# Kernel tuning notes

Hardware: AMD Instinct MI355X
Metric: run time of the kernel (lower is better)

## Reference

```python
import jax, jax.numpy as jnp
import numpy as np

N = 50000          # nodes
E = 800000         # edges (before self-loops)
F_IN = 256         # feature_dim
HEADS = 3
OUT = 128          # per-head channels
HO = HEADS * OUT   # 384
NUM_GRAPHS = 64
NUM_CLASSES = 2
SLOPE = 0.2        # PyG GATConv default negative_slope


def setup_inputs() -> dict:
    key = jax.random.key(0)
    ks = jax.random.split(key, 8)
    x = jax.random.normal(ks[0], (N, F_IN), dtype=jnp.float32)
    edge_index = jax.random.randint(ks[1], (2, E), 0, N)
    batch = jnp.sort(jax.random.randint(ks[2], (N,), 0, NUM_GRAPHS))
    # GATConv params (glorot-ish scales)
    W = jax.random.normal(ks[3], (F_IN, HO), dtype=jnp.float32) * (1.0 / np.sqrt(F_IN))
    att_src = jax.random.normal(ks[4], (HEADS, OUT), dtype=jnp.float32) * 0.1
    att_dst = jax.random.normal(ks[5], (HEADS, OUT), dtype=jnp.float32) * 0.1
    bias = jnp.zeros((HO,), dtype=jnp.float32)
    fc_w = jax.random.normal(ks[6], (HO, NUM_CLASSES), dtype=jnp.float32) * 0.05
    fc_b = jnp.zeros((NUM_CLASSES,), dtype=jnp.float32)
    return {"x": x, "edge_index": edge_index, "batch": batch, "W": W,
            "att_src": att_src, "att_dst": att_dst, "bias": bias,
            "fc_w": fc_w, "fc_b": fc_b}


def reference(x, edge_index, batch, W, att_src, att_dst, bias, fc_w, fc_b):
    n = x.shape[0]
    h = (x @ W).reshape(n, HEADS, OUT)                      # [N, H, C]
    # add self-loops (PyG default add_self_loops=True)
    loops = jnp.arange(n)
    src = jnp.concatenate([edge_index[0], loops])           # [E+N]
    dst = jnp.concatenate([edge_index[1], loops])
    # per-node attention logits
    a_src = jnp.einsum('nhc,hc->nh', h, att_src)            # [N, H]
    a_dst = jnp.einsum('nhc,hc->nh', h, att_dst)
    e = jax.nn.leaky_relu(a_src[src] + a_dst[dst], SLOPE)   # [E+N, H]
    # segment softmax over incoming edges of each dst node
    emax = jax.ops.segment_max(e, dst, num_segments=n)
    ex = jnp.exp(e - emax[dst])
    denom = jax.ops.segment_sum(ex, dst, num_segments=n)
    alpha = ex / (denom[dst] + 1e-16)                       # [E+N, H]
    # weighted scatter-add aggregation
    msg = h[src] * alpha[:, :, None]                        # [E+N, H, C]
    out = jax.ops.segment_sum(msg, dst, num_segments=n)     # [N, H, C]
    out = jax.nn.relu(out.reshape(n, HO) + bias)            # [N, 384]
    # global mean pool per graph
    counts = jax.ops.segment_sum(jnp.ones((n,), out.dtype), batch,
                                 num_segments=NUM_GRAPHS)
    pooled = jax.ops.segment_sum(out, batch, num_segments=NUM_GRAPHS)
    pooled = pooled / jnp.maximum(counts, 1.0)[:, None]     # [G, 384]
    return pooled @ fc_w + fc_b                             # [G, num_classes]
```

## Files before the change

kernel.cpp:

```cpp
#include <hip/hip_runtime.h>
#include <hip/hip_bf16.h>
#include <math.h>

#define HEADS 3
#define HO 384
#define NGRAPH 64
#define F_IN 256
#define SLOPE 0.2f

typedef __attribute__((ext_vector_type(8))) short bf8;
typedef __attribute__((ext_vector_type(4))) float f4;

__device__ __forceinline__ unsigned short bfr(float f) {
    unsigned u = __float_as_uint(f);
    u += 0x7fffu + ((u >> 16) & 1u);
    return (unsigned short)(u >> 16);
}
__device__ __forceinline__ float bflo(unsigned u) { return __uint_as_float(u << 16); }
__device__ __forceinline__ float bfhi(unsigned u) { return __uint_as_float(u & 0xffff0000u); }
__device__ __forceinline__ float lrelu(float v) { return (v > 0.f) ? v : SLOPE * v; }

__global__ __launch_bounds__(256) void misc_k(const int* __restrict__ ei,
                                              const float* __restrict__ W,
                                              const int* __restrict__ batch,
                                              int* __restrict__ count,
                                              int* __restrict__ rank,
                                              short* __restrict__ WbT,
                                              int* __restrict__ gstart,
                                              int NBc, int E, int N) {
    int b = blockIdx.x;
    if (b < NBc) {
        int e = b * 256 + threadIdx.x;
        int ET = E + N;
        if (e >= ET) return;
        int d = (e < E) ? ei[E + e] : (e - E);
        rank[e] = atomicAdd(&count[d], 1);
    } else if (b < NBc + 384) {
        int n = b - NBc;
        int k = threadIdx.x;
        WbT[n * 256 + k] = (short)bfr(W[(size_t)k * HO + n]);
    } else {
        int g = threadIdx.x;
        if (g > NGRAPH) return;
        int lo = 0, hi = N;
        while (lo < hi) { int mid = (lo + hi) >> 1; if (batch[mid] < g) lo = mid + 1; else hi = mid; }
        gstart[g] = lo;
    }
}

#define XS_STRIDE 40
__global__ __launch_bounds__(256, 3) void gemm_att(const float* __restrict__ X,
                                                   const short* __restrict__ WbT,
                                                   const float* __restrict__ att_src,
                                                   const float* __restrict__ att_dst,
                                                   unsigned* __restrict__ Hb,
                                                   float* __restrict__ aSrcO,
                                                   float* __restrict__ aDstO, int N) {
    __shared__ short Xs[64 * XS_STRIDE];
    __shared__ short Bs[384 * XS_STRIDE];
    __shared__ float lsS[64][8];
    __shared__ float lsD[64][8];
    int t = threadIdx.x;
    int w = t >> 6, lane = t & 63;
    int quad = lane >> 4, l15 = lane & 15;
    int rbase = blockIdx.x * 64;

    int sr = t >> 2;
    int sko = (t & 3) * 8;
    int xrow = rbase + sr;
    xrow = (xrow < N) ? xrow : (N - 1);
    const float* xrp = X + (size_t)xrow * F_IN;

    f4 acc[4][6] = {};

    float4 p0 = *(const float4*)(xrp + sko);
    float4 p1 = *(const float4*)(xrp + sko + 4);

    for (int k0 = 0; k0 < F_IN; k0 += 32) {
        __syncthreads();
        {
            bf8 pk;
            pk[0] = (short)bfr(p0.x); pk[1] = (short)bfr(p0.y);
            pk[2] = (short)bfr(p0.z); pk[3] = (short)bfr(p0.w);
            pk[4] = (short)bfr(p1.x); pk[5] = (short)bfr(p1.y);
            pk[6] = (short)bfr(p1.z); pk[7] = (short)bfr(p1.w);
            *(bf8*)(&Xs[sr * XS_STRIDE + sko]) = pk;
        }
#pragma unroll
        for (int i = 0; i < 6; i++) {
            int n = i * 64 + sr;
            bf8 b = *(const bf8*)(WbT + (size_t)n * F_IN + k0 + sko);
            *(bf8*)(&Bs[n * XS_STRIDE + sko]) = b;
        }
        __syncthreads();
        if (k0 + 32 < F_IN) {
            p0 = *(const float4*)(xrp + k0 + 32 + sko);
            p1 = *(const float4*)(xrp + k0 + 32 + sko + 4);
        }
        bf8 ar[4], br[6];
#pragma unroll
        for (int at = 0; at < 4; at++)
            ar[at] = *(const bf8*)(&Xs[(at * 16 + l15) * XS_STRIDE + quad * 8]);
#pragma unroll
        for (int nt = 0; nt < 6; nt++)
            br[nt] = *(const bf8*)(&Bs[(w * 96 + nt * 16 + l15) * XS_STRIDE + quad * 8]);
#pragma unroll
        for (int at = 0; at < 4; at++)
#pragma unroll
            for (int nt = 0; nt < 6; nt++)
                acc[at][nt] = __builtin_amdgcn_mfma_f32_16x16x32_bf16(ar[at], br[nt], acc[at][nt], 0, 0, 0);
    }

    const int splits[4] = {6, 2, 4, 0};
    int split = splits[w];
    float asv[6], adv[6];
#pragma unroll
    for (int nt = 0; nt < 6; nt++) {
        int c = w * 96 + nt * 16 + l15;
        asv[nt] = att_src[c];
        adv[nt] = att_dst[c];
    }
#pragma unroll
    for (int at = 0; at < 4; at++) {
#pragma unroll
        for (int r = 0; r < 4; r++) {
            float paS = 0.f, pbS = 0.f, paD = 0.f, pbD = 0.f;
#pragma unroll
            for (int nt = 0; nt < 6; nt++) {
                float v = acc[at][nt][r];
                if (nt < split) { paS += v * asv[nt]; paD += v * adv[nt]; }
                else            { pbS += v * asv[nt]; pbD += v * adv[nt]; }
            }
#pragma unroll
            for (int off = 1; off < 16; off <<= 1) {
                paS += __shfl_xor(paS, off); pbS += __shfl_xor(pbS, off);
                paD += __shfl_xor(paD, off); pbD += __shfl_xor(pbD, off);
            }
            if (l15 == 0) {
                int row = at * 16 + quad * 4 + r;
                lsS[row][w * 2 + 0] = paS; lsS[row][w * 2 + 1] = pbS;
                lsD[row][w * 2 + 0] = paD; lsD[row][w * 2 + 1] = pbD;
            }
        }
    }
#pragma unroll
    for (int at = 0; at < 4; at++) {
#pragma unroll
        for (int nt = 0; nt < 6; nt++) {
#pragma unroll
            for (int r = 0; r < 4; r++) {
                float v = acc[at][nt][r];
                float vp = __shfl_xor(v, 1);
                int node = rbase + at * 16 + quad * 4 + r;
                if (!(lane & 1) && node < N) {
                    unsigned pk = (unsigned)bfr(v) | ((unsigned)bfr(vp) << 16);
                    Hb[(size_t)node * 192 + w * 48 + nt * 8 + (l15 >> 1)] = pk;
                }
            }
        }
    }
    __syncthreads();
    if (t < 64) {
        int node = rbase + t;
        if (node < N) {
            aSrcO[node * 3 + 0] = lsS[t][0] + lsS[t][2];
            aSrcO[node * 3 + 1] = lsS[t][3] + lsS[t][4];
            aSrcO[node * 3 + 2] = lsS[t][5] + lsS[t][7];
            aDstO[node * 3 + 0] = lsD[t][0] + lsD[t][2];
            aDstO[node * 3 + 1] = lsD[t][3] + lsD[t][4];
            aDstO[node * 3 + 2] = lsD[t][5] + lsD[t][7];
        }
    }
}

__global__ __launch_bounds__(256) void scan_a(const int* __restrict__ count,
                                              int* __restrict__ offsets,
                                              int* __restrict__ bsums, int N) {
    __shared__ int tmp[256];
    int t = threadIdx.x;
    int i = blockIdx.x * 256 + t;
    int v = (i < N) ? count[i] : 0;
    tmp[t] = v;
    __syncthreads();
    for (int off = 1; off < 256; off <<= 1) {
        int x = (t >= off) ? tmp[t - off] : 0;
        __syncthreads();
        tmp[t] += x;
        __syncthreads();
    }
    if (i < N) offsets[i] = tmp[t] - v;
    if (t == 255) bsums[blockIdx.x] = tmp[255];
}

__global__ __launch_bounds__(256) void scan_b(int* __restrict__ bsums, int NB) {
    __shared__ int tmp[256];
    int t = threadIdx.x;
    int v = (t < NB) ? bsums[t] : 0;
    tmp[t] = v;
    __syncthreads();
    for (int off = 1; off < 256; off <<= 1) {
        int x = (t >= off) ? tmp[t - off] : 0;
        __syncthreads();
        tmp[t] += x;
        __syncthreads();
    }
    if (t < NB) bsums[t] = tmp[t] - v;
}

__global__ __launch_bounds__(256) void scan_c(int* __restrict__ offsets,
                                              const int* __restrict__ bsums, int N) {
    int i = blockIdx.x * 256 + threadIdx.x;
    if (i < N) offsets[i] += bsums[blockIdx.x];
}

__global__ __launch_bounds__(256) void scatter_k(const int* __restrict__ ei,
                                                 const int* __restrict__ rank,
                                                 const int* __restrict__ offsets,
                                                 int* __restrict__ csr_src, int E, int N) {
    int e = blockIdx.x * 256 + threadIdx.x;
    int ET = E + N;
    if (e >= ET) return;
    int s, d;
    if (e < E) { s = ei[e]; d = ei[E + e]; } else { s = e - E; d = s; }
    csr_src[offsets[d] + rank[e]] = s;
}

__global__ __launch_bounds__(256) void aggregate_k(const unsigned* __restrict__ Hb,
                                                   const int* __restrict__ csr_src,
                                                   const int* __restrict__ offsets,
                                                   const int* __restrict__ count,
                                                   const float* __restrict__ a_src,
                                                   const float* __restrict__ a_dst,
                                                   const float* __restrict__ bias,
                                                   unsigned* __restrict__ outb, int N) {
    int wid = blockIdx.x * 4 + (threadIdx.x >> 6);
    int lane = threadIdx.x & 63;
    if (wid >= N) return;
    int start = offsets[wid], n = count[wid];
    float ad0 = a_dst[wid * 3 + 0], ad1 = a_dst[wid * 3 + 1], ad2 = a_dst[wid * 3 + 2];
    float a0l = 0.f, a0h = 0.f, a1l = 0.f, a1h = 0.f, a2l = 0.f, a2h = 0.f;

    if (n <= 64) {
        int sreg = 0;
        float l0 = -INFINITY, l1 = -INFINITY, l2 = -INFINITY;
        if (lane < n) {
            sreg = csr_src[start + lane];
            l0 = lrelu(a_src[sreg * 3 + 0] + ad0);
            l1 = lrelu(a_src[sreg * 3 + 1] + ad1);
            l2 = lrelu(a_src[sreg * 3 + 2] + ad2);
        }
        unsigned u0[8], u1[8], u2[8];
#pragma unroll
        for (int q = 0; q < 8; q++) {
            int s = __shfl(sreg, q);
            const unsigned* h = Hb + (size_t)s * 192;
            u0[q] = h[lane]; u1[q] = h[lane + 64]; u2[q] = h[lane + 128];
        }
        float m0 = l0, m1 = l1, m2 = l2;
#pragma unroll
        for (int off = 1; off < 64; off <<= 1) {
            m0 = fmaxf(m0, __shfl_xor(m0, off));
            m1 = fmaxf(m1, __shfl_xor(m1, off));
            m2 = fmaxf(m2, __shfl_xor(m2, off));
        }
        float e0 = (lane < n) ? expf(l0 - m0) : 0.f;
        float e1 = (lane < n) ? expf(l1 - m1) : 0.f;
        float e2 = (lane < n) ? expf(l2 - m2) : 0.f;
        float s0 = e0, s1 = e1, s2 = e2;
#pragma unroll
        for (int off = 1; off < 64; off <<= 1) {
            s0 += __shfl_xor(s0, off);
            s1 += __shfl_xor(s1, off);
            s2 += __shfl_xor(s2, off);
        }
        float i0 = 1.f / (s0 + 1e-16f), i1 = 1.f / (s1 + 1e-16f), i2 = 1.f / (s2 + 1e-16f);
        for (int j = 0; j < n; j += 8) {
            float wq0[8], wq1[8], wq2[8];
#pragma unroll
            for (int q = 0; q < 8; q++) {
                wq0[q] = __shfl(e0, j + q);
                wq1[q] = __shfl(e1, j + q);
                wq2[q] = __shfl(e2, j + q);
            }
#pragma unroll
            for (int q = 0; q < 8; q++) {
                a0l += wq0[q] * bflo(u0[q]); a0h += wq0[q] * bfhi(u0[q]);
                a1l += wq1[q] * bflo(u1[q]); a1h += wq1[q] * bfhi(u1[q]);
                a2l += wq2[q] * bflo(u2[q]); a2h += wq2[q] * bfhi(u2[q]);
            }
            if (j + 8 < n) {
#pragma unroll
                for (int q = 0; q < 8; q++) {
                    int s = __shfl(sreg, j + 8 + q);
                    const unsigned* h = Hb + (size_t)s * 192;
                    u0[q] = h[lane]; u1[q] = h[lane + 64]; u2[q] = h[lane + 128];
                }
            }
        }
        a0l *= i0; a0h *= i0;
        a1l *= i1; a1h *= i1;
        a2l *= i2; a2h *= i2;
    } else {
        float m0 = -INFINITY, m1 = -INFINITY, m2 = -INFINITY;
        for (int j = lane; j < n; j += 64) {
            int s = csr_src[start + j];
            m0 = fmaxf(m0, lrelu(a_src[s * 3 + 0] + ad0));
            m1 = fmaxf(m1, lrelu(a_src[s * 3 + 1] + ad1));
            m2 = fmaxf(m2, lrelu(a_src[s * 3 + 2] + ad2));
        }
#pragma unroll
        for (int off = 1; off < 64; off <<= 1) {
            m0 = fmaxf(m0, __shfl_xor(m0, off));
            m1 = fmaxf(m1, __shfl_xor(m1, off));
            m2 = fmaxf(m2, __shfl_xor(m2, off));
        }
        float s0 = 0.f, s1 = 0.f, s2 = 0.f;
        for (int j = lane; j < n; j += 64) {
            int s = csr_src[start + j];
            s0 += expf(lrelu(a_src[s * 3 + 0] + ad0) - m0);
            s1 += expf(lrelu(a_src[s * 3 + 1] + ad1) - m1);
            s2 += expf(lrelu(a_src[s * 3 + 2] + ad2) - m2);
        }
#pragma unroll
        for (int off = 1; off < 64; off <<= 1) {
            s0 += __shfl_xor(s0, off);
            s1 += __shfl_xor(s1, off);
            s2 += __shfl_xor(s2, off);
        }
        float i0 = 1.f / (s0 + 1e-16f), i1 = 1.f / (s1 + 1e-16f), i2 = 1.f / (s2 + 1e-16f);
        for (int j = 0; j < n; j++) {
            int s = csr_src[start + j];
            float w0 = expf(lrelu(a_src[s * 3 + 0] + ad0) - m0) * i0;
            float w1 = expf(lrelu(a_src[s * 3 + 1] + ad1) - m1) * i1;
            float w2 = expf(lrelu(a_src[s * 3 + 2] + ad2) - m2) * i2;
            const unsigned* h = Hb + (size_t)s * 192;
            unsigned u0 = h[lane], u1 = h[lane + 64], u2 = h[lane + 128];
            a0l += w0 * bflo(u0); a0h += w0 * bfhi(u0);
            a1l += w1 * bflo(u1); a1h += w1 * bfhi(u1);
            a2l += w2 * bflo(u2); a2h += w2 * bfhi(u2);
        }
    }

    unsigned* orow = outb + (size_t)wid * 192;
    int c0 = 2 * lane;
    float b0 = bias[c0], b1 = bias[c0 + 1];
    float b2 = bias[128 + c0], b3 = bias[128 + c0 + 1];
    float b4 = bias[256 + c0], b5 = bias[256 + c0 + 1];
    float v, x0, x1;
    unsigned pk;
    v = a0l + b0; x0 = (v > 0.f) ? v : 0.f;
    v = a0h + b1; x1 = (v > 0.f) ? v : 0.f;
    pk = (unsigned)bfr(x0) | ((unsigned)bfr(x1) << 16);
    orow[lane] = pk;
    v = a1l + b2; x0 = (v > 0.f) ? v : 0.f;
    v = a1h + b3; x1 = (v > 0.f) ? v : 0.f;
    pk = (unsigned)bfr(x0) | ((unsigned)bfr(x1) << 16);
    orow[64 + lane] = pk;
    v = a2l + b4; x0 = (v > 0.f) ? v : 0.f;
    v = a2h + b5; x1 = (v > 0.f) ? v : 0.f;
    pk = (unsigned)bfr(x0) | ((unsigned)bfr(x1) << 16);
    orow[128 + lane] = pk;
}

__global__ __launch_bounds__(192) void pool_k(const unsigned* __restrict__ outb,
                                              const int* __restrict__ gstart,
                                              float* __restrict__ pooled) {
    int g = blockIdx.x;
    int chunk = blockIdx.y;
    int t = threadIdx.x;
    int lo = gstart[g], hi = gstart[g + 1];
    float al = 0.f, ah = 0.f;
    for (int r = lo + chunk; r < hi; r += 8) {
        unsigned u = outb[(size_t)r * 192 + t];
        al += bflo(u);
        ah += bfhi(u);
    }
    atomicAdd(&pooled[g * HO + 2 * t], al);
    atomicAdd(&pooled[g * HO + 2 * t + 1], ah);
}

__global__ __launch_bounds__(64) void fc_k(const float* __restrict__ pooled,
                                           const int* __restrict__ gstart,
                                           const float* __restrict__ fc_w,
                                           const float* __restrict__ fc_b,
                                           float* __restrict__ out) {
    int g = blockIdx.x;
    int lane = threadIdx.x;
    float a0 = 0.f, a1 = 0.f;
#pragma unroll
    for (int k = 0; k < 6; k++) {
        int c = lane + 64 * k;
        float pv = pooled[g * HO + c];
        a0 += pv * fc_w[c * 2 + 0];
        a1 += pv * fc_w[c * 2 + 1];
    }
#pragma unroll
    for (int off = 32; off > 0; off >>= 1) {
        a0 += __shfl_down(a0, off);
        a1 += __shfl_down(a1, off);
    }
    if (lane == 0) {
        float cnt = fmaxf((float)(gstart[g + 1] - gstart[g]), 1.0f);
        out[g * 2 + 0] = a0 / cnt + fc_b[0];
        out[g * 2 + 1] = a1 / cnt + fc_b[1];
    }
}

extern "C" void kernel_launch(void* const* d_in, const int* in_sizes, int n_in,
                              void* d_out, int out_size, void* d_ws, size_t ws_size,
                              hipStream_t stream) {
    const float* x       = (const float*)d_in[0];
    const int*   ei      = (const int*)d_in[1];
    const int*   batch   = (const int*)d_in[2];
    const float* W       = (const float*)d_in[3];
    const float* att_src = (const float*)d_in[4];
    const float* att_dst = (const float*)d_in[5];
    const float* bias    = (const float*)d_in[6];
    const float* fc_w    = (const float*)d_in[7];
    const float* fc_b    = (const float*)d_in[8];
    float* out = (float*)d_out;

    const int N = in_sizes[2];
    const int E = in_sizes[1] / 2;
    const int ET = E + N;

    char* p = (char*)d_ws;
    auto alloc = [&](size_t bytes) -> char* {
        char* r = p;
        p += (bytes + 255) & ~(size_t)255;
        return r;
    };
    short*    wbt    = (short*)alloc((size_t)HO * F_IN * 2);
    unsigned* hb     = (unsigned*)alloc((size_t)N * 192 * 4);
    unsigned* outb   = (unsigned*)alloc((size_t)N * 192 * 4);
    float*    a_src  = (float*)alloc((size_t)N * 3 * 4);
    float*    a_dst  = (float*)alloc((size_t)N * 3 * 4);
    char*     zstart = p;
    int*      count  = (int*)alloc((size_t)N * 4);
    float*    pooled = (float*)alloc((size_t)NGRAPH * HO * 4);
    size_t    zbytes = (size_t)(p - zstart);
    int*      offsets = (int*)alloc((size_t)N * 4);
    int*      rank    = (int*)alloc((size_t)ET * 4);
    int*      bsums   = (int*)alloc(4096);
    int*      gstart  = (int*)alloc(1024);
    int*      csr_src = (int*)alloc((size_t)ET * 4);

    hipMemsetAsync(zstart, 0, zbytes, stream);

    int NBc = (ET + 255) / 256;
    misc_k<<<NBc + 384 + 1, 256, 0, stream>>>(ei, W, batch, count, rank, wbt, gstart,
                                              NBc, E, N);
    gemm_att<<<(N + 63) / 64, 256, 0, stream>>>(x, wbt, att_src, att_dst,
                                                hb, a_src, a_dst, N);
    int NB = (N + 255) / 256;
    scan_a<<<NB, 256, 0, stream>>>(count, offsets, bsums, N);
    scan_b<<<1, 256, 0, stream>>>(bsums, NB);
    scan_c<<<NB, 256, 0, stream>>>(offsets, bsums, N);
    scatter_k<<<(ET + 255) / 256, 256, 0, stream>>>(ei, rank, offsets, csr_src, E, N);
    aggregate_k<<<(N + 3) / 4, 256, 0, stream>>>(hb, csr_src, offsets, count,
                                                 a_src, a_dst, bias, outb, N);
    dim3 pg(NGRAPH, 8);
    pool_k<<<pg, 192, 0, stream>>>(outb, gstart, pooled);
    fc_k<<<NGRAPH, 64, 0, stream>>>(pooled, gstart, fc_w, fc_b, out);

    (void)n_in; (void)out_size; (void)ws_size;
}
```

Measured before the change: 330.0 us.

## Quantize projected node features to int8 with per-node-per-head scales for aggregation

The GEMM epilogue now computes a per-node, per-head absmax and stores the projected features as int8 instead of bf16. The per-head scales are packed alongside the source attention logits in an 8-float record per node. The aggregation kernel gathers half as many bytes per neighbour row, folds the dequant scale into the softmax weight, and writes output with wider vector stores using 48 lanes. This cuts the gather traffic that dominates aggregation, in exchange for int8 quantization error and extra unpack arithmetic per element.

```diff
diff --git a/kernel.cpp b/kernel.cpp
--- a/kernel.cpp
+++ b/kernel.cpp
@@ -10,6 +10,8 @@
 
 typedef __attribute__((ext_vector_type(8))) short bf8;
 typedef __attribute__((ext_vector_type(4))) float f4;
+typedef __attribute__((ext_vector_type(2))) unsigned u2v;
+typedef __attribute__((ext_vector_type(4))) unsigned u4v;
 
 __device__ __forceinline__ unsigned short bfr(float f) {
     unsigned u = __float_as_uint(f);
@@ -19,6 +21,17 @@
 __device__ __forceinline__ float bflo(unsigned u) { return __uint_as_float(u << 16); }
 __device__ __forceinline__ float bfhi(unsigned u) { return __uint_as_float(u & 0xffff0000u); }
 __device__ __forceinline__ float lrelu(float v) { return (v > 0.f) ? v : SLOPE * v; }
+
+__device__ __forceinline__ void dec_fma(float* acc, float wm, unsigned ux, unsigned uy) {
+    acc[0] += wm * (float)((signed char)(ux));
+    acc[1] += wm * (float)((signed char)(ux >> 8));
+    acc[2] += wm * (float)((signed char)(ux >> 16));
+    acc[3] += wm * (float)((signed char)(ux >> 24));
+    acc[4] += wm * (float)((signed char)(uy));
+    acc[5] += wm * (float)((signed char)(uy >> 8));
+    acc[6] += wm * (float)((signed char)(uy >> 16));
+    acc[7] += wm * (float)((signed char)(uy >> 24));
+}
 
 __global__ __launch_bounds__(256) void misc_k(const int* __restrict__ ei,
                                               const float* __restrict__ W,
@@ -53,13 +66,15 @@
                                                    const short* __restrict__ WbT,
                                                    const float* __restrict__ att_src,
                                                    const float* __restrict__ att_dst,
-                                                   unsigned* __restrict__ Hb,
-                                                   float* __restrict__ aSrcO,
+                                                   signed char* __restrict__ hc,
+                                                   float* __restrict__ ni,
                                                    float* __restrict__ aDstO, int N) {
     __shared__ short Xs[64 * XS_STRIDE];
     __shared__ short Bs[384 * XS_STRIDE];
     __shared__ float lsS[64][8];
     __shared__ float lsD[64][8];
+    __shared__ float lsM[64][8];
+    __shared__ float sclS[64][4];
     int t = threadIdx.x;
     int w = t >> 6, lane = t & 63;
     int quad = lane >> 4, l15 = lane & 15;
@@ -146,29 +161,63 @@
 #pragma unroll
     for (int at = 0; at < 4; at++) {
 #pragma unroll
-        for (int nt = 0; nt < 6; nt++) {
-#pragma unroll
-            for (int r = 0; r < 4; r++) {
-                float v = acc[at][nt][r];
-                float vp = __shfl_xor(v, 1);
-                int node = rbase + at * 16 + quad * 4 + r;
-                if (!(lane & 1) && node < N) {
-                    unsigned pk = (unsigned)bfr(v) | ((unsigned)bfr(vp) << 16);
-                    Hb[(size_t)node * 192 + w * 48 + nt * 8 + (l15 >> 1)] = pk;
-                }
+        for (int r = 0; r < 4; r++) {
+            float pa = 0.f, pb = 0.f;
+#pragma unroll
+            for (int nt = 0; nt < 6; nt++) {
+                float v = fabsf(acc[at][nt][r]);
+                if (nt < split) pa = fmaxf(pa, v); else pb = fmaxf(pb, v);
+            }
+#pragma unroll
+            for (int off = 1; off < 16; off <<= 1) {
+                pa = fmaxf(pa, __shfl_xor(pa, off));
+                pb = fmaxf(pb, __shfl_xor(pb, off));
+            }
+            if (l15 == 0) {
+                int row = at * 16 + quad * 4 + r;
+                lsM[row][w * 2 + 0] = pa; lsM[row][w * 2 + 1] = pb;
             }
         }
     }
     __syncthreads();
     if (t < 64) {
+        float s0 = fmaxf(lsM[t][0], lsM[t][2]);
+        float s1 = fmaxf(lsM[t][3], lsM[t][4]);
+        float s2 = fmaxf(lsM[t][5], lsM[t][7]);
+        sclS[t][0] = (s0 > 0.f) ? 127.f / s0 : 0.f;
+        sclS[t][1] = (s1 > 0.f) ? 127.f / s1 : 0.f;
+        sclS[t][2] = (s2 > 0.f) ? 127.f / s2 : 0.f;
         int node = rbase + t;
         if (node < N) {
-            aSrcO[node * 3 + 0] = lsS[t][0] + lsS[t][2];
-            aSrcO[node * 3 + 1] = lsS[t][3] + lsS[t][4];
-            aSrcO[node * 3 + 2] = lsS[t][5] + lsS[t][7];
             aDstO[node * 3 + 0] = lsD[t][0] + lsD[t][2];
             aDstO[node * 3 + 1] = lsD[t][3] + lsD[t][4];
             aDstO[node * 3 + 2] = lsD[t][5] + lsD[t][7];
+            float4 nA, nB;
+            nA.x = lsS[t][0] + lsS[t][2];
+            nA.y = lsS[t][3] + lsS[t][4];
+            nA.z = lsS[t][5] + lsS[t][7];
+            nA.w = s0 / 127.f;
+            nB.x = s1 / 127.f;
+            nB.y = s2 / 127.f;
+            nB.z = 0.f; nB.w = 0.f;
+            *(float4*)(ni + (size_t)node * 8) = nA;
+            *(float4*)(ni + (size_t)node * 8 + 4) = nB;
+        }
+    }
+    __syncthreads();
+#pragma unroll
+    for (int at = 0; at < 4; at++) {
+#pragma unroll
+        for (int nt = 0; nt < 6; nt++) {
+            int hd = (w * 96 + nt * 16) >> 7;
+#pragma unroll
+            for (int r = 0; r < 4; r++) {
+                int row = at * 16 + quad * 4 + r;
+                int node = rbase + row;
+                float rq = sclS[row][hd];
+                int qi = (int)rintf(acc[at][nt][r] * rq);
+                if (node < N) hc[(size_t)node * 384 + w * 96 + nt * 16 + l15] = (signed char)qi;
+            }
         }
     }
 }
@@ -225,11 +274,11 @@
     csr_src[offsets[d] + rank[e]] = s;
 }
 
-__global__ __launch_bounds__(256) void aggregate_k(const unsigned* __restrict__ Hb,
+__global__ __launch_bounds__(256) void aggregate_k(const unsigned* __restrict__ hcw,
                                                    const int* __restrict__ csr_src,
                                                    const int* __restrict__ offsets,
                                                    const int* __restrict__ count,
-                                                   const float* __restrict__ a_src,
+                                                   const float* __restrict__ ni,
                                                    const float* __restrict__ a_dst,
                                                    const float* __restrict__ bias,
                                                    unsigned* __restrict__ outb, int N) {
@@ -238,128 +287,118 @@
     if (wid >= N) return;
     int start = offsets[wid], n = count[wid];
     float ad0 = a_dst[wid * 3 + 0], ad1 = a_dst[wid * 3 + 1], ad2 = a_dst[wid * 3 + 2];
-    float a0l = 0.f, a0h = 0.f, a1l = 0.f, a1h = 0.f, a2l = 0.f, a2h = 0.f;
+    int head_my = lane >> 4;
+    int off = (lane < 48) ? 2 * lane : 0;
+    float acc[8] = {0.f, 0.f, 0.f, 0.f, 0.f, 0.f, 0.f, 0.f};
+    float i0, i1, i2;
 
     if (n <= 64) {
         int sreg = 0;
         float l0 = -INFINITY, l1 = -INFINITY, l2 = -INFINITY;
+        float s0v = 0.f, s1v = 0.f, s2v = 0.f;
         if (lane < n) {
             sreg = csr_src[start + lane];
-            l0 = lrelu(a_src[sreg * 3 + 0] + ad0);
-            l1 = lrelu(a_src[sreg * 3 + 1] + ad1);
-            l2 = lrelu(a_src[sreg * 3 + 2] + ad2);
-        }
-        unsigned u0[8], u1[8], u2[8];
-#pragma unroll
-        for (int q = 0; q < 8; q++) {
-            int s = __shfl(sreg, q);
-            const unsigned* h = Hb + (size_t)s * 192;
-            u0[q] = h[lane]; u1[q] = h[lane + 64]; u2[q] = h[lane + 128];
+            float4 A = *(const float4*)(ni + (size_t)sreg * 8);
+            float4 B = *(const float4*)(ni + (size_t)sreg * 8 + 4);
+            l0 = lrelu(A.x + ad0); l1 = lrelu(A.y + ad1); l2 = lrelu(A.z + ad2);
+            s0v = A.w; s1v = B.x; s2v = B.y;
         }
         float m0 = l0, m1 = l1, m2 = l2;
 #pragma unroll
-        for (int off = 1; off < 64; off <<= 1) {
-            m0 = fmaxf(m0, __shfl_xor(m0, off));
-            m1 = fmaxf(m1, __shfl_xor(m1, off));
-            m2 = fmaxf(m2, __shfl_xor(m2, off));
+        for (int o = 1; o < 64; o <<= 1) {
+            m0 = fmaxf(m0, __shfl_xor(m0, o));
+            m1 = fmaxf(m1, __shfl_xor(m1, o));
+            m2 = fmaxf(m2, __shfl_xor(m2, o));
         }
         float e0 = (lane < n) ? expf(l0 - m0) : 0.f;
         float e1 = (lane < n) ? expf(l1 - m1) : 0.f;
         float e2 = (lane < n) ? expf(l2 - m2) : 0.f;
         float s0 = e0, s1 = e1, s2 = e2;
 #pragma unroll
-        for (int off = 1; off < 64; off <<= 1) {
-            s0 += __shfl_xor(s0, off);
-            s1 += __shfl_xor(s1, off);
-            s2 += __shfl_xor(s2, off);
-        }
-        float i0 = 1.f / (s0 + 1e-16f), i1 = 1.f / (s1 + 1e-16f), i2 = 1.f / (s2 + 1e-16f);
+        for (int o = 1; o < 64; o <<= 1) {
+            s0 += __shfl_xor(s0, o);
+            s1 += __shfl_xor(s1, o);
+            s2 += __shfl_xor(s2, o);
+        }
+        i0 = 1.f / (s0 + 1e-16f); i1 = 1.f / (s1 + 1e-16f); i2 = 1.f / (s2 + 1e-16f);
+        float f0 = e0 * s0v, f1 = e1 * s1v, f2 = e2 * s2v;
+
         for (int j = 0; j < n; j += 8) {
-            float wq0[8], wq1[8], wq2[8];
+            unsigned ux[8], uy[8];
 #pragma unroll
             for (int q = 0; q < 8; q++) {
-                wq0[q] = __shfl(e0, j + q);
-                wq1[q] = __shfl(e1, j + q);
-                wq2[q] = __shfl(e2, j + q);
+                int s = __shfl(sreg, j + q);
+                u2v u = *(const u2v*)(hcw + (size_t)s * 96 + off);
+                ux[q] = u.x; uy[q] = u.y;
             }
 #pragma unroll
             for (int q = 0; q < 8; q++) {
-                a0l += wq0[q] * bflo(u0[q]); a0h += wq0[q] * bfhi(u0[q]);
-                a1l += wq1[q] * bflo(u1[q]); a1h += wq1[q] * bfhi(u1[q]);
-                a2l += wq2[q] * bflo(u2[q]); a2h += wq2[q] * bfhi(u2[q]);
-            }
-            if (j + 8 < n) {
-#pragma unroll
-                for (int q = 0; q < 8; q++) {
-                    int s = __shfl(sreg, j + 8 + q);
-                    const unsigned* h = Hb + (size_t)s * 192;
-                    u0[q] = h[lane]; u1[q] = h[lane + 64]; u2[q] = h[lane + 128];
-                }
-            }
-        }
-        a0l *= i0; a0h *= i0;
-        a1l *= i1; a1h *= i1;
-        a2l *= i2; a2h *= i2;
+                float w0 = __shfl(f0, j + q);
+                float w1 = __shfl(f1, j + q);
+                float w2 = __shfl(f2, j + q);
+                float wm = (head_my == 0) ? w0 : ((head_my == 1) ? w1 : w2);
+                dec_fma(acc, wm, ux[q], uy[q]);
+            }
+        }
     } else {
         float m0 = -INFINITY, m1 = -INFINITY, m2 = -INFINITY;
         for (int j = lane; j < n; j += 64) {
             int s = csr_src[start + j];
-            m0 = fmaxf(m0, lrelu(a_src[s * 3 + 0] + ad0));
-            m1 = fmaxf(m1, lrelu(a_src[s * 3 + 1] + ad1));
-            m2 = fmaxf(m2, lrelu(a_src[s * 3 + 2] + ad2));
-        }
-#pragma unroll
-        for (int off = 1; off < 64; off <<= 1) {
-            m0 = fmaxf(m0, __shfl_xor(m0, off));
-            m1 = fmaxf(m1, __shfl_xor(m1, off));
-            m2 = fmaxf(m2, __shfl_xor(m2, off));
+            float4 A = *(const float4*)(ni + (size_t)s * 8);
+            m0 = fmaxf(m0, lrelu(A.x + ad0));
+            m1 = fmaxf(m1, lrelu(A.y + ad1));
+            m2 = fmaxf(m2, lrelu(A.z + ad2));
+        }
+#pragma unroll
+        for (int o = 1; o < 64; o <<= 1) {
+            m0 = fmaxf(m0, __shfl_xor(m0, o));
+            m1 = fmaxf(m1, __shfl_xor(m1, o));
+            m2 = fmaxf(m2, __shfl_xor(m2, o));
         }
         float s0 = 0.f, s1 = 0.f, s2 = 0.f;
         for (int j = lane; j < n; j += 64) {
             int s = csr_src[start + j];
-            s0 += expf(lrelu(a_src[s * 3 + 0] + ad0) - m0);
-            s1 += expf(lrelu(a_src[s * 3 + 1] + ad1) - m1);
-            s2 += expf(lrelu(a_src[s * 3 + 2] + ad2) - m2);
-        }
-#pragma unroll
-        for (int off = 1; off < 64; off <<= 1) {
-            s0 += __shfl_xor(s0, off);
-            s1 += __shfl_xor(s1, off);
-            s2 += __shfl_xor(s2, off);
-        }
-        float i0 = 1.f / (s0 + 1e-16f), i1 = 1.f / (s1 + 1e-16f), i2 = 1.f / (s2 + 1e-16f);
+            float4 A = *(const float4*)(ni + (size_t)s * 8);
+            s0 += expf(lrelu(A.x + ad0) - m0);
+            s1 += expf(lrelu(A.y + ad1) - m1);
+            s2 += expf(lrelu(A.z + ad2) - m2);
+        }
+#pragma unroll
+        for (int o = 1; o < 64; o <<= 1) {
+            s0 += __shfl_xor(s0, o);
+            s1 += __shfl_xor(s1, o);
+            s2 += __shfl_xor(s2, o);
+        }
+        i0 = 1.f / (s0 + 1e-16f); i1 = 1.f / (s1 + 1e-16f); i2 = 1.f / (s2 + 1e-16f);
         for (int j = 0; j < n; j++) {
             int s = csr_src[start + j];
-            float w0 = expf(lrelu(a_src[s * 3 + 0] + ad0) - m0) * i0;
-            float w1 = expf(lrelu(a_src[s * 3 + 1] + ad1) - m1) * i1;
-            float w2 = expf(lrelu(a_src[s * 3 + 2] + ad2) - m2) * i2;
-            const unsigned* h = Hb + (size_t)s * 192;
-            unsigned u0 = h[lane], u1 = h[lane + 64], u2 = h[lane + 128];
-            a0l += w0 * bflo(u0); a0h += w0 * bfhi(u0);
-            a1l += w1 * bflo(u1); a1h += w1 * bfhi(u1);
-            a2l += w2 * bflo(u2); a2h += w2 * bfhi(u2);
-        }
-    }
-
-    unsigned* orow = outb + (size_t)wid * 192;
-    int c0 = 2 * lane;
-    float b0 = bias[c0], b1 = bias[c0 + 1];
-    float b2 = bias[128 + c0], b3 = bias[128 + c0 + 1];
-    float b4 = bias[256 + c0], b5 = bias[256 + c0 + 1];
-    float v, x0, x1;
-    unsigned pk;
-    v = a0l + b0; x0 = (v > 0.f) ? v : 0.f;
-    v = a0h + b1; x1 = (v > 0.f) ? v : 0.f;
-    pk = (unsigned)bfr(x0) | ((unsigned)bfr(x1) << 16);
-    orow[lane] = pk;
-    v = a1l + b2; x0 = (v > 0.f) ? v : 0.f;
-    v = a1h + b3; x1 = (v > 0.f) ? v : 0.f;
-    pk = (unsigned)bfr(x0) | ((unsigned)bfr(x1) << 16);
-    orow[64 + lane] = pk;
-    v = a2l + b4; x0 = (v > 0.f) ? v : 0.f;
-    v = a2h + b5; x1 = (v > 0.f) ? v : 0.f;
-    pk = (unsigned)bfr(x0) | ((unsigned)bfr(x1) << 16);
-    orow[128 + lane] = pk;
+            float4 A = *(const float4*)(ni + (size_t)s * 8);
+            float4 B = *(const float4*)(ni + (size_t)s * 8 + 4);
+            float w0 = expf(lrelu(A.x + ad0) - m0) * A.w;
+            float w1 = expf(lrelu(A.y + ad1) - m1) * B.x;
+            float w2 = expf(lrelu(A.z + ad2) - m2) * B.y;
+            float wm = (head_my == 0) ? w0 : ((head_my == 1) ? w1 : w2);
+            u2v u = *(const u2v*)(hcw + (size_t)s * 96 + off);
+            dec_fma(acc, wm, u.x, u.y);
+        }
+    }
+
+    if (lane < 48) {
+        float im = ((head_my == 0) ? i0 : (head_my == 1) ? i1 : i2);
+        float4 b0 = *(const float4*)(bias + 8 * lane);
+        float4 b1 = *(const float4*)(bias + 8 * lane + 4);
+        float bb[8] = {b0.x, b0.y, b0.z, b0.w, b1.x, b1.y, b1.z, b1.w};
+        u4v pk;
+#pragma unroll
+        for (int j = 0; j < 4; j++) {
+            float x0 = acc[2 * j] * im + bb[2 * j];
+            float x1 = acc[2 * j + 1] * im + bb[2 * j + 1];
+            x0 = (x0 > 0.f) ? x0 : 0.f;
+            x1 = (x1 > 0.f) ? x1 : 0.f;
+            pk[j] = (unsigned)bfr(x0) | ((unsigned)bfr(x1) << 16);
+        }
+        *(u4v*)(outb + (size_t)wid * 192 + 4 * lane) = pk;
+    }
 }
 
 __global__ __launch_bounds__(192) void pool_k(const unsigned* __restrict__ outb,
@@ -430,20 +469,20 @@
         p += (bytes + 255) & ~(size_t)255;
         return r;
     };
-    short*    wbt    = (short*)alloc((size_t)HO * F_IN * 2);
-    unsigned* hb     = (unsigned*)alloc((size_t)N * 192 * 4);
-    unsigned* outb   = (unsigned*)alloc((size_t)N * 192 * 4);
-    float*    a_src  = (float*)alloc((size_t)N * 3 * 4);
-    float*    a_dst  = (float*)alloc((size_t)N * 3 * 4);
-    char*     zstart = p;
-    int*      count  = (int*)alloc((size_t)N * 4);
-    float*    pooled = (float*)alloc((size_t)NGRAPH * HO * 4);
-    size_t    zbytes = (size_t)(p - zstart);
-    int*      offsets = (int*)alloc((size_t)N * 4);
-    int*      rank    = (int*)alloc((size_t)ET * 4);
-    int*      bsums   = (int*)alloc(4096);
-    int*      gstart  = (int*)alloc(1024);
-    int*      csr_src = (int*)alloc((size_t)ET * 4);
+    short*       wbt    = (short*)alloc((size_t)HO * F_IN * 2);
+    signed char* hc     = (signed char*)alloc((size_t)N * 384);
+    unsigned*    outb   = (unsigned*)alloc((size_t)N * 192 * 4);
+    float*       ni     = (float*)alloc((size_t)N * 8 * 4);
+    float*       a_dst  = (float*)alloc((size_t)N * 3 * 4);
+    char*        zstart = p;
+    int*         count  = (int*)alloc((size_t)N * 4);
+    float*       pooled = (float*)alloc((size_t)NGRAPH * HO * 4);
+    size_t       zbytes = (size_t)(p - zstart);
+    int*         offsets = (int*)alloc((size_t)N * 4);
+    int*         rank    = (int*)alloc((size_t)ET * 4);
+    int*         bsums   = (int*)alloc(4096);
+    int*         gstart  = (int*)alloc(1024);
+    int*         csr_src = (int*)alloc((size_t)ET * 4);
 
     hipMemsetAsync(zstart, 0, zbytes, stream);
 
@@ -451,14 +490,14 @@
     misc_k<<<NBc + 384 + 1, 256, 0, stream>>>(ei, W, batch, count, rank, wbt, gstart,
                                               NBc, E, N);
     gemm_att<<<(N + 63) / 64, 256, 0, stream>>>(x, wbt, att_src, att_dst,
-                                                hb, a_src, a_dst, N);
+                                                hc, ni, a_dst, N);
     int NB = (N + 255) / 256;
     scan_a<<<NB, 256, 0, stream>>>(count, offsets, bsums, N);
     scan_b<<<1, 256, 0, stream>>>(bsums, NB);
     scan_c<<<NB, 256, 0, stream>>>(offsets, bsums, N);
     scatter_k<<<(ET + 255) / 256, 256, 0, stream>>>(ei, rank, offsets, csr_src, E, N);
-    aggregate_k<<<(N + 3) / 4, 256, 0, stream>>>(hb, csr_src, offsets, count,
-                                                 a_src, a_dst, bias, outb, N);
+    aggregate_k<<<(N + 3) / 4, 256, 0, stream>>>((const unsigned*)hc, csr_src, offsets,
+                                                 count, ni, a_dst, bias, outb, N);
     dim3 pg(NGRAPH, 8);
     pool_k<<<pg, 192, 0, stream>>>(outb, gstart, pooled);
     fc_k<<<NGRAPH, 64, 0, stream>>>(pooled, gstart, fc_w, fc_b, out);
```

New measurement: 312.7 us. 1.06x faster.
